# Performance work log

Measured on AMD Instinct MI355X. Metric: run time of the kernel, lower is better.

The kernel has to match this reference:

```python
import jax, jax.numpy as jnp
import numpy as np

L = 2          # conv layers
N = 50000      # nodes
E = 800000     # edges (before self loops)
F_IN = 256     # raw node features
C = 32         # embed features (out_channels per head)
H = 4          # heads
HC = H * C
ED = 1         # edge feature dim
EPS = 1e-5
NEG_SLOPE = 0.2


def _xavier(k, shape):
    fan_in, fan_out = shape[-2], shape[-1]
    lim = float(np.sqrt(6.0 / (fan_in + fan_out)))
    return jax.random.uniform(k, shape, jnp.float32, -lim, lim)


def setup_inputs() -> dict:
    key = jax.random.key(0)
    ks = jax.random.split(key, 12)
    x = jax.random.normal(ks[0], (N, F_IN), jnp.float32)
    src = jax.random.randint(ks[1], (E,), 0, N, dtype=jnp.int32)
    off = jax.random.randint(ks[2], (E,), 1, N, dtype=jnp.int32)
    dst = (src + off) % N  # guarantees no pre-existing self loops (PyG removes then re-adds them)
    edge_index = jnp.stack([src, dst])
    edge_attr = jax.random.normal(ks[3], (E, ED), jnp.float32)
    return {
        "x": x,
        "edge_index": edge_index,
        "edge_attr": edge_attr,
        "W_emb": _xavier(ks[4], (F_IN, C)),
        "b_emb": jnp.zeros((C,), jnp.float32),
        "ln0_w": jnp.ones((C,), jnp.float32),
        "ln0_b": jnp.zeros((C,), jnp.float32),
        "Wl": _xavier(ks[5], (L, C, HC)),
        "bl": jnp.zeros((L, HC), jnp.float32),
        "Wr": _xavier(ks[6], (L, C, HC)),
        "br": jnp.zeros((L, HC), jnp.float32),
        "We": _xavier(ks[7], (L, ED, HC)),
        "att": jax.random.normal(ks[8], (L, H, C), jnp.float32) * 0.1,
        "gat_b": jnp.zeros((L, HC), jnp.float32),
        "ln1_w": jnp.ones((L, HC), jnp.float32),
        "ln1_b": jnp.zeros((L, HC), jnp.float32),
        "lin_w": _xavier(ks[9], (L, HC, C)),
        "lin_b": jnp.zeros((L, C), jnp.float32),
        "ln2_w": jnp.ones((L, C), jnp.float32),
        "ln2_b": jnp.zeros((L, C), jnp.float32),
    }


def _node_ln(x, w, b):
    # torch.nn.LayerNorm over last dim
    mu = jnp.mean(x, axis=-1, keepdims=True)
    xc = x - mu
    var = jnp.mean(xc * xc, axis=-1, keepdims=True)
    return xc / jnp.sqrt(var + EPS) * w + b


def _graph_ln(x, w, b):
    # torch_geometric.nn.norm.LayerNorm, mode='graph': normalize over ALL nodes+features
    mu = jnp.mean(x)
    xc = x - mu
    var = jnp.mean(xc * xc)
    return xc / jnp.sqrt(var + EPS) * w + b


def _gatv2_layer(h, src, dst, ea, Wl, bl, Wr, br, We, att, gat_b):
    n = h.shape[0]
    xl = (h @ Wl + bl).reshape(n, H, C)   # lin_l(x) -> source transform
    xr = (h @ Wr + br).reshape(n, H, C)   # lin_r(x) -> target transform
    e = (ea @ We).reshape(-1, H, C)       # lin_edge(edge_attr), no bias
    z = jax.nn.leaky_relu(xl[src] + xr[dst] + e, NEG_SLOPE)   # [Etot,H,C]
    logits = jnp.einsum("ehc,hc->eh", z, att)                  # [Etot,H]
    # segment softmax over destination nodes (every node has a self loop)
    m = jax.ops.segment_max(logits, dst, num_segments=n)
    ex = jnp.exp(logits - m[dst])
    s = jax.ops.segment_sum(ex, dst, num_segments=n)
    alpha = ex / s[dst]                                        # [Etot,H]
    msg = alpha[..., None] * xl[src]                           # [Etot,H,C]
    out = jax.ops.segment_sum(msg, dst, num_segments=n)        # [N,H,C]
    return out.reshape(n, HC) + gat_b


def reference(x, edge_index, edge_attr, W_emb, b_emb, ln0_w, ln0_b, Wl, bl, Wr, br,
              We, att, gat_b, ln1_w, ln1_b, lin_w, lin_b, ln2_w, ln2_b):
    n = x.shape[0]
    loop = jnp.arange(n, dtype=edge_index.dtype)
    src = jnp.concatenate([edge_index[0], loop])
    dst = jnp.concatenate([edge_index[1], loop])
    ea = jnp.concatenate([edge_attr, jnp.zeros((n, edge_attr.shape[1]), edge_attr.dtype)])  # fill_value=0.0

    # node_embed: Dropout(eval=identity) -> Linear -> LayerNorm -> ReLU
    h = jax.nn.relu(_node_ln(x @ W_emb + b_emb, ln0_w, ln0_b))
    hs = [h]
    for i in range(L):
        g = _gatv2_layer(h, src, dst, ea, Wl[i], bl[i], Wr[i], br[i], We[i], att[i], gat_b[i])
        g = jax.nn.relu(_graph_ln(g, ln1_w[i], ln1_b[i]))     # PyG graph-mode LayerNorm + ReLU
        g = g @ lin_w[i] + lin_b[i]                            # heads>1 projection back to C
        h = jax.nn.relu(_node_ln(g, ln2_w[i], ln2_b[i]))
        hs.append(h)
    # JumpingKnowledge mode='max': elementwise max over layer outputs
    return jnp.max(jnp.stack(hs, axis=0), axis=0)
```

## Files before the change

### kernel.cpp

```cpp
#include <hip/hip_runtime.h>
#include <hip/hip_fp16.h>

constexpr int kNodes = 50000;
constexpr int kNE    = 800000;
constexpr int kFin   = 256;
constexpr int kC     = 32;
constexpr int kH     = 4;
constexpr int kHC    = 128;
constexpr int kTN    = 16;
constexpr int kEmbedBlocks = kNodes / kTN;
constexpr int kTransBlocks = (kNodes + 31) / 32;
constexpr int kHistGS = 256;
constexpr int kReoGS  = 256;
constexpr int kDegBlocks = (kNodes + 255) / 256;
constexpr float kEps   = 1e-5f;
constexpr float kSlope = 0.2f;
constexpr float kL2E   = 1.44269504f;
constexpr float kShift2 = 8.0f * 1.44269504f;

typedef _Float16 f16;
typedef _Float16 f16x2 __attribute__((ext_vector_type(2)));
typedef _Float16 f16x4 __attribute__((ext_vector_type(4)));
struct alignas(16) h8 { f16x2 v[4]; };

__device__ __forceinline__ float fdot2_(f16x2 a, f16x2 b, float c) {
#if __has_builtin(__builtin_amdgcn_fdot2)
    return __builtin_amdgcn_fdot2(a, b, c, false);
#else
    return fmaf((float)a.x, (float)b.x, fmaf((float)a.y, (float)b.y, c));
#endif
}

template<int CTRL>
__device__ __forceinline__ float dpp_add(float v) {
    int x = __builtin_amdgcn_update_dpp(0, __float_as_int(v), CTRL, 0xF, 0xF, true);
    return v + __int_as_float(x);
}
__device__ __forceinline__ float red8(float p) {
    p = dpp_add<0xB1>(p);
    p = dpp_add<0x4E>(p);
    p = dpp_add<0x141>(p);
    return p;
}

__global__ void __launch_bounds__(256) k_prep(
    unsigned* __restrict__ deg, const float* __restrict__ W, f16* __restrict__ Wh,
    const float* __restrict__ linw, f16* __restrict__ lwh, float* __restrict__ stats) {
    int t = threadIdx.x;
    if (blockIdx.x == 0 && t < 4) stats[t] = 0.f;
    if (blockIdx.x < kDegBlocks) {
        int i = blockIdx.x * 256 + t;
        if (i < kNodes) deg[i] = 0u;
        return;
    }
    int bi = blockIdx.x - kDegBlocks;
    if (bi < 32) {
        int i = bi * 256 + t;
        int k = i >> 5, c = i & 31;
        Wh[((k >> 3) * kC + c) * 8 + (k & 7)] = (f16)W[i];
        return;
    }
    bi -= 32;
    int i = bi * 256 + t;
    int l = i >> 12, il = i & 4095;
    int k = il >> 5, c = il & 31;
    lwh[l * 4096 + ((k >> 3) * kC + c) * 8 + (k & 7)] = (f16)linw[i];
}

__global__ void __launch_bounds__(256) k_embed_hist(
    const float* __restrict__ x, const f16* __restrict__ Wh, const float* __restrict__ b,
    const float* __restrict__ lnw, const float* __restrict__ lnb,
    float* __restrict__ h, float* __restrict__ jk,
    const int* __restrict__ dst, int* __restrict__ deg, unsigned short* __restrict__ rank) {
    __shared__ f16 sxh[kTN * kFin];
    __shared__ f16 sWh[kFin / 8 * kC * 8];
    int t = threadIdx.x;
    if (blockIdx.x < kHistGS) {
        const int stride = kHistGS * 256;
        int e = blockIdx.x * 256 + t;
        for (; e + 3 * stride < kNE; e += 4 * stride) {
            int d0 = dst[e], d1 = dst[e + stride], d2 = dst[e + 2 * stride], d3 = dst[e + 3 * stride];
            int r0 = atomicAdd(&deg[d0], 1);
            int r1 = atomicAdd(&deg[d1], 1);
            int r2 = atomicAdd(&deg[d2], 1);
            int r3 = atomicAdd(&deg[d3], 1);
            rank[e] = (unsigned short)r0;
            rank[e + stride] = (unsigned short)r1;
            rank[e + 2 * stride] = (unsigned short)r2;
            rank[e + 3 * stride] = (unsigned short)r3;
        }
        for (; e < kNE; e += stride) {
            int d = dst[e];
            rank[e] = (unsigned short)atomicAdd(&deg[d], 1);
        }
        return;
    }
    int n0 = (blockIdx.x - kHistGS) * kTN;
    {
        const h8* Wg = (const h8*)Wh;
        h8* sW8 = (h8*)sWh;
        for (int i = t; i < kFin * kC / 8; i += 256) sW8[i] = Wg[i];
    }
    const float4* xg4 = (const float4*)(x + (long)n0 * kFin);
    f16x4* sx4 = (f16x4*)sxh;
    for (int i = t; i < kTN * kFin / 4; i += 256) {
        float4 v = xg4[i];
        f16x4 hv; hv.x = (f16)v.x; hv.y = (f16)v.y; hv.z = (f16)v.z; hv.w = (f16)v.w;
        sx4[i] = hv;
    }
    __syncthreads();
    int c = t & 31, n2 = t >> 5;
    const h8* xa = (const h8*)(sxh + n2 * kFin);
    const h8* xb = (const h8*)(sxh + (n2 + 8) * kFin);
    const h8* wr = (const h8*)sWh;
    float a0 = 0.f, a0b = 0.f, a1 = 0.f, a1b = 0.f;
    #pragma unroll 8
    for (int i8 = 0; i8 < kFin / 8; ++i8) {
        h8 xv0 = xa[i8];
        h8 xv1 = xb[i8];
        h8 wv  = wr[i8 * kC + c];
        a0  = fdot2_(xv0.v[0], wv.v[0], a0);
        a0b = fdot2_(xv0.v[1], wv.v[1], a0b);
        a0  = fdot2_(xv0.v[2], wv.v[2], a0);
        a0b = fdot2_(xv0.v[3], wv.v[3], a0b);
        a1  = fdot2_(xv1.v[0], wv.v[0], a1);
        a1b = fdot2_(xv1.v[1], wv.v[1], a1b);
        a1  = fdot2_(xv1.v[2], wv.v[2], a1);
        a1b = fdot2_(xv1.v[3], wv.v[3], a1b);
    }
    float acc0 = a0 + a0b, acc1 = a1 + a1b;
    float bc = b[c], lw = lnw[c], lb = lnb[c];
    {
        float y = acc0 + bc;
        float m = y;
        #pragma unroll
        for (int o = 1; o < 32; o <<= 1) m += __shfl_xor(m, o);
        m *= (1.f / kC);
        float xc = y - m, v = xc * xc;
        #pragma unroll
        for (int o = 1; o < 32; o <<= 1) v += __shfl_xor(v, o);
        v *= (1.f / kC);
        float out = fmaxf(xc * rsqrtf(v + kEps) * lw + lb, 0.f);
        int node = n0 + n2;
        h[node * kC + c] = out;
        jk[node * kC + c] = out;
    }
    {
        float y = acc1 + bc;
        float m = y;
        #pragma unroll
        for (int o = 1; o < 32; o <<= 1) m += __shfl_xor(m, o);
        m *= (1.f / kC);
        float xc = y - m, v = xc * xc;
        #pragma unroll
        for (int o = 1; o < 32; o <<= 1) v += __shfl_xor(v, o);
        v *= (1.f / kC);
        float out = fmaxf(xc * rsqrtf(v + kEps) * lw + lb, 0.f);
        int node = n0 + n2 + 8;
        h[node * kC + c] = out;
        jk[node * kC + c] = out;
    }
}

__device__ __forceinline__ void trans_body(
    int bid, float* s_h, const float* __restrict__ h,
    const float* __restrict__ Wl, const float* __restrict__ bl,
    const float* __restrict__ Wr, const float* __restrict__ br,
    __half* __restrict__ xl, float* __restrict__ xr) {
    int t = threadIdx.x;
    int j = t & 127, hf = t >> 7;
    float wl[kC], wr[kC];
    #pragma unroll
    for (int k = 0; k < kC; ++k) { wl[k] = Wl[k * kHC + j]; wr[k] = Wr[k * kHC + j]; }
    float blj = bl[j], brj = br[j];
    int n0 = bid * 32;
    int nn = min(32, kNodes - n0);
    for (int i = t; i < nn * kC; i += 256) s_h[i] = h[n0 * kC + i];
    __syncthreads();
    int nend = min(nn, hf * 16 + 16);
    for (int n = hf * 16; n < nend; ++n) {
        const float4* h4 = (const float4*)(s_h + n * kC);
        float al = blj, ar = brj;
        #pragma unroll
        for (int kq = 0; kq < 8; ++kq) {
            float4 hv = h4[kq];
            al += hv.x * wl[kq*4] + hv.y * wl[kq*4+1] + hv.z * wl[kq*4+2] + hv.w * wl[kq*4+3];
            ar += hv.x * wr[kq*4] + hv.y * wr[kq*4+1] + hv.z * wr[kq*4+2] + hv.w * wr[kq*4+3];
        }
        long g = (long)(n0 + n) * kHC + j;
        xl[g] = __float2half(al);
        xr[g] = ar;
    }
}

__global__ void __launch_bounds__(256) k_trans_reorder(
    const float* __restrict__ h,
    const float* __restrict__ Wl, const float* __restrict__ bl,
    const float* __restrict__ Wr, const float* __restrict__ br,
    __half* __restrict__ xl, float* __restrict__ xr,
    const int* __restrict__ src, const int* __restrict__ dst, const float* __restrict__ ea,
    const int* __restrict__ rowptr, const unsigned short* __restrict__ rank,
    int2* __restrict__ epack) {
    __shared__ float s_h[32 * kC];
    if (blockIdx.x < kReoGS) {
        const int stride = kReoGS * 256;
        int e = blockIdx.x * 256 + threadIdx.x;
        for (; e + 3 * stride < kNE; e += 4 * stride) {
            int e1 = e + stride, e2 = e + 2 * stride, e3 = e + 3 * stride;
            int d0 = dst[e], d1 = dst[e1], d2 = dst[e2], d3 = dst[e3];
            int r0 = rank[e], r1 = rank[e1], r2 = rank[e2], r3 = rank[e3];
            int p0 = rowptr[d0] + r0, p1 = rowptr[d1] + r1;
            int p2 = rowptr[d2] + r2, p3 = rowptr[d3] + r3;
            epack[p0] = make_int2(src[e],  __float_as_int(ea[e]));
            epack[p1] = make_int2(src[e1], __float_as_int(ea[e1]));
            epack[p2] = make_int2(src[e2], __float_as_int(ea[e2]));
            epack[p3] = make_int2(src[e3], __float_as_int(ea[e3]));
        }
        for (; e < kNE; e += stride) {
            int d = dst[e];
            int pos = rowptr[d] + (int)rank[e];
            epack[pos] = make_int2(src[e], __float_as_int(ea[e]));
        }
        return;
    }
    trans_body(blockIdx.x - kReoGS, s_h, h, Wl, bl, Wr, br, xl, xr);
}

__global__ void __launch_bounds__(256) k_scan1(const int* __restrict__ deg,
                                               int* __restrict__ excl, int* __restrict__ bsum) {
    __shared__ int s[256];
    int t = threadIdx.x;
    int i = blockIdx.x * 256 + t;
    int v = (i < kNodes) ? deg[i] : 0;
    s[t] = v;
    __syncthreads();
    for (int o = 1; o < 256; o <<= 1) {
        int tv = (t >= o) ? s[t - o] : 0;
        __syncthreads();
        s[t] += tv;
        __syncthreads();
    }
    if (i < kNodes) excl[i] = s[t] - v;
    if (t == 255) bsum[blockIdx.x] = s[255];
}

__global__ void __launch_bounds__(256) k_scan2(int* __restrict__ bsum, int nb) {
    __shared__ int s[256];
    int t = threadIdx.x;
    int v = (t < nb) ? bsum[t] : 0;
    s[t] = v;
    __syncthreads();
    for (int o = 1; o < 256; o <<= 1) {
        int tv = (t >= o) ? s[t - o] : 0;
        __syncthreads();
        s[t] += tv;
        __syncthreads();
    }
    if (t < nb) bsum[t] = s[t];
}

__global__ void __launch_bounds__(256) k_scan3(int* __restrict__ excl, const int* __restrict__ bsum) {
    int i = blockIdx.x * 256 + threadIdx.x;
    if (i >= kNodes) return;
    if (blockIdx.x > 0) excl[i] += bsum[blockIdx.x - 1];
}

struct h4 { __half2 a, b; };
template<int U>
__device__ __forceinline__ void gat_batch(
    const int2* __restrict__ epack, int base2, bool slot0, int f,
    const h4* __restrict__ xl4, float4 Wev, float4 xrv, float4 av,
    float& l, float& o0, float& o1, float& o2, float& o3) {
    int2 pa[U], pb[U];
    #pragma unroll
    for (int u = 0; u < U; ++u) {
        pa[u] = epack[base2 + 2 * u];
        pb[u] = epack[base2 + 2 * u + 1];
    }
    h4 xv[U]; float eav[U];
    #pragma unroll
    for (int u = 0; u < U; ++u) {
        int srow = slot0 ? pa[u].x : pb[u].x;
        xv[u] = xl4[(long)srow * 32 + f];
        eav[u] = __int_as_float(slot0 ? pa[u].y : pb[u].y);
    }
    #pragma unroll
    for (int u = 0; u < U; ++u) {
        float2 x01 = __half22float2(xv[u].a), x23 = __half22float2(xv[u].b);
        float a0 = fmaf(eav[u], Wev.x, xrv.x) + x01.x;
        float a1 = fmaf(eav[u], Wev.y, xrv.y) + x01.y;
        float a2 = fmaf(eav[u], Wev.z, xrv.z) + x23.x;
        float a3 = fmaf(eav[u], Wev.w, xrv.w) + x23.y;
        a0 = fmaxf(a0, kSlope * a0); a1 = fmaxf(a1, kSlope * a1);
        a2 = fmaxf(a2, kSlope * a2); a3 = fmaxf(a3, kSlope * a3);
        float pp = red8(a0 * av.x + a1 * av.y + a2 * av.z + a3 * av.w);
        float eu = __builtin_amdgcn_exp2f(pp - kShift2);
        l += eu;
        o0 = fmaf(eu, x01.x, o0); o1 = fmaf(eu, x01.y, o1);
        o2 = fmaf(eu, x23.x, o2); o3 = fmaf(eu, x23.y, o3);
    }
}

__global__ void __launch_bounds__(256) k_edge(
    const int* __restrict__ rowptr, const int* __restrict__ deg,
    const int2* __restrict__ epack,
    const __half* __restrict__ xl, float* __restrict__ xrg,
    const float* __restrict__ We, const float* __restrict__ att,
    const float* __restrict__ gat_b, float* __restrict__ ps, float* __restrict__ pq) {
    int t = threadIdx.x & 63;
    int w = __builtin_amdgcn_readfirstlane(threadIdx.x >> 6);
    int d = blockIdx.x * 4 + w;
    int f = t & 31;
    bool slot0 = (t < 32);
    float em0 = slot0 ? 1.f : 0.f;

    const h4* xl4 = (const h4*)xl;
    long rowq = (long)d * 32;

    float4 xrv = ((const float4*)xrg)[rowq + f];
    float4 Wev = ((const float4*)We)[f];
    float4 av  = ((const float4*)att)[f];
    av.x *= kL2E; av.y *= kL2E; av.z *= kL2E; av.w *= kL2E;
    float4 gb  = ((const float4*)gat_b)[f];

    h4 xs = xl4[rowq + f];
    float2 xs01 = __half22float2(xs.a), xs23 = __half22float2(xs.b);

    float z0 = xs01.x + xrv.x, z1 = xs01.y + xrv.y;
    float z2 = xs23.x + xrv.z, z3 = xs23.y + xrv.w;
    z0 = fmaxf(z0, kSlope * z0); z1 = fmaxf(z1, kSlope * z1);
    z2 = fmaxf(z2, kSlope * z2); z3 = fmaxf(z3, kSlope * z3);
    float p = red8(z0 * av.x + z1 * av.y + z2 * av.z + z3 * av.w);
    float ee = __builtin_amdgcn_exp2f(p - kShift2) * em0;
    float l = ee;
    float o0 = ee * xs01.x, o1 = ee * xs01.y, o2 = ee * xs23.x, o3 = ee * xs23.y;

    int base = rowptr[d], cnt = deg[d];
    int npair = cnt >> 1;
    int e = 0;
    for (; e + 8 <= npair; e += 8)
        gat_batch<8>(epack, base + 2 * e, slot0, f, xl4, Wev, xrv, av, l, o0, o1, o2, o3);
    if (e + 4 <= npair) {
        gat_batch<4>(epack, base + 2 * e, slot0, f, xl4, Wev, xrv, av, l, o0, o1, o2, o3);
        e += 4;
    }
    for (; e < npair; ++e)
        gat_batch<1>(epack, base + 2 * e, slot0, f, xl4, Wev, xrv, av, l, o0, o1, o2, o3);
    if (cnt & 1) {
        int2 ep = epack[base + cnt - 1];
        int srow = ep.x;
        float eav = __int_as_float(ep.y);
        h4 xv = xl4[(long)srow * 32 + f];
        float2 x01 = __half22float2(xv.a), x23 = __half22float2(xv.b);
        float a0 = fmaf(eav, Wev.x, xrv.x) + x01.x;
        float a1 = fmaf(eav, Wev.y, xrv.y) + x01.y;
        float a2 = fmaf(eav, Wev.z, xrv.z) + x23.x;
        float a3 = fmaf(eav, Wev.w, xrv.w) + x23.y;
        a0 = fmaxf(a0, kSlope * a0); a1 = fmaxf(a1, kSlope * a1);
        a2 = fmaxf(a2, kSlope * a2); a3 = fmaxf(a3, kSlope * a3);
        float pp = red8(a0 * av.x + a1 * av.y + a2 * av.z + a3 * av.w);
        float eu = __builtin_amdgcn_exp2f(pp - kShift2) * em0;
        l += eu;
        o0 = fmaf(eu, x01.x, o0); o1 = fmaf(eu, x01.y, o1);
        o2 = fmaf(eu, x23.x, o2); o3 = fmaf(eu, x23.y, o3);
    }
    l  += __shfl_xor(l, 32);
    o0 += __shfl_xor(o0, 32); o1 += __shfl_xor(o1, 32);
    o2 += __shfl_xor(o2, 32); o3 += __shfl_xor(o3, 32);
    float rl = __builtin_amdgcn_rcpf(l);
    float v0 = o0 * rl, v1 = o1 * rl, v2 = o2 * rl, v3 = o3 * rl;
    if (slot0)
        ((float4*)xrg)[rowq + f] = make_float4(v0, v1, v2, v3);
    float vb0 = v0 + gb.x, vb1 = v1 + gb.y, vb2 = v2 + gb.z, vb3 = v3 + gb.w;
    float s = vb0 + vb1 + vb2 + vb3;
    float q = vb0 * vb0 + vb1 * vb1 + vb2 * vb2 + vb3 * vb3;
    #pragma unroll
    for (int mm = 1; mm < 32; mm <<= 1) { s += __shfl_xor(s, mm); q += __shfl_xor(q, mm); }
    if (t == 0) { ps[d] = s; pq[d] = q; }
}

__global__ void __launch_bounds__(1024) k_statsr(
    const float* __restrict__ ps, const float* __restrict__ pq, float* __restrict__ stats) {
    __shared__ float rs[1024], rq[1024];
    int t = threadIdx.x;
    float s = 0.f, q = 0.f;
    for (int i = blockIdx.x * 1024 + t; i < kNodes; i += 8 * 1024) { s += ps[i]; q += pq[i]; }
    rs[t] = s; rq[t] = q;
    __syncthreads();
    for (int o = 512; o > 0; o >>= 1) {
        if (t < o) { rs[t] += rs[t + o]; rq[t] += rq[t + o]; }
        __syncthreads();
    }
    if (t == 0) { atomicAdd(&stats[0], rs[0]); atomicAdd(&stats[1], rq[0]); }
}

__global__ void __launch_bounds__(256) k_post(
    const float* __restrict__ g, const float* __restrict__ gat_b,
    const float* __restrict__ ln1w, const float* __restrict__ ln1b,
    const f16* __restrict__ lwh, const float* __restrict__ linb,
    const float* __restrict__ ln2w, const float* __restrict__ ln2b,
    const float* __restrict__ stats, const float* __restrict__ jk_in,
    float* __restrict__ jk_out, int do_trans,
    const float* __restrict__ Wl, const float* __restrict__ bl,
    const float* __restrict__ Wr, const float* __restrict__ br,
    __half* __restrict__ xl, float* __restrict__ xr) {
    __shared__ __align__(16) char smem[17408];
    float* s_hh  = (float*)smem;
    f16*   s_lwh = (f16*)(smem + 1024);
    f16*   s_vbh = (f16*)(smem + 9216);
    int t = threadIdx.x;
    int n0 = blockIdx.x * 8;
    int j = t & 127;
    const float inv = 1.f / ((float)kNodes * kHC);
    float mean = stats[0] * inv;
    float var  = stats[1] * inv - mean * mean;
    float rstd = rsqrtf(var + kEps);
    {
        const h8* Wg = (const h8*)lwh;
        h8* sW8 = (h8*)s_lwh;
        for (int i = t; i < kHC * kC / 8; i += 256) sW8[i] = Wg[i];
    }
    for (int i = t; i < 8 * kHC; i += 256) {
        int node = n0 + (i >> 7), f = i & 127;
        float a = (g[(long)node * kHC + f] + gat_b[f] - mean) * rstd * ln1w[f] + ln1b[f];
        s_vbh[i] = (f16)fmaxf(a, 0.f);
    }
    __syncthreads();
    int n = t >> 5, c = t & 31;
    int node = n0 + n;
    const h8* vb8 = (const h8*)(s_vbh + n * kHC);
    const h8* w8  = (const h8*)s_lwh;
    float a0 = 0.f, a0b = 0.f;
    #pragma unroll
    for (int k8 = 0; k8 < kHC / 8; ++k8) {
        h8 vv = vb8[k8];
        h8 wv = w8[k8 * kC + c];
        a0  = fdot2_(vv.v[0], wv.v[0], a0);
        a0b = fdot2_(vv.v[1], wv.v[1], a0b);
        a0  = fdot2_(vv.v[2], wv.v[2], a0);
        a0b = fdot2_(vv.v[3], wv.v[3], a0b);
    }
    float acc = linb[c] + a0 + a0b;
    float m = acc;
    #pragma unroll
    for (int mm = 1; mm < 32; mm <<= 1) m += __shfl_xor(m, mm);
    m *= (1.f / kC);
    float dd = acc - m;
    float q = dd * dd;
    #pragma unroll
    for (int mm = 1; mm < 32; mm <<= 1) q += __shfl_xor(q, mm);
    q *= (1.f / kC);
    float out = dd * rsqrtf(q + kEps) * ln2w[c] + ln2b[c];
    out = fmaxf(out, 0.f);
    jk_out[node * kC + c] = fmaxf(jk_in[node * kC + c], out);
    if (!do_trans) return;
    s_hh[n * kC + c] = out;
    __syncthreads();
    f16x2* w2 = (f16x2*)(smem + 1024);
    for (int i = t; i < kC * kHC; i += 256) {
        f16x2 pw; pw.x = (f16)Wl[i]; pw.y = (f16)Wr[i];
        w2[i] = pw;
    }
    __syncthreads();
    float wl[kC], wr[kC];
    #pragma unroll
    for (int k = 0; k < kC; ++k) {
        f16x2 pw = w2[k * kHC + j];
        wl[k] = (float)pw.x; wr[k] = (float)pw.y;
    }
    int hf = t >> 7;
    float blj = bl[j], brj = br[j];
    #pragma unroll
    for (int nn2 = 0; nn2 < 4; ++nn2) {
        int nn = hf * 4 + nn2;
        const float4* h4p = (const float4*)(s_hh + nn * kC);
        float al = blj, ar = brj;
        #pragma unroll
        for (int kq = 0; kq < 8; ++kq) {
            float4 hv = h4p[kq];
            al += hv.x * wl[kq*4] + hv.y * wl[kq*4+1] + hv.z * wl[kq*4+2] + hv.w * wl[kq*4+3];
            ar += hv.x * wr[kq*4] + hv.y * wr[kq*4+1] + hv.z * wr[kq*4+2] + hv.w * wr[kq*4+3];
        }
        long gg = (long)(n0 + nn) * kHC + j;
        xl[gg] = __float2half(al);
        xr[gg] = ar;
    }
}

extern "C" void kernel_launch(void* const* d_in, const int* in_sizes, int n_in,
                              void* d_out, int out_size, void* d_ws, size_t ws_size,
                              hipStream_t stream) {
    (void)in_sizes; (void)n_in; (void)out_size; (void)ws_size;
    const float* x     = (const float*)d_in[0];
    const int*   ei    = (const int*)d_in[1];
    const int*   src   = ei;
    const int*   dst   = ei + kNE;
    const float* ea    = (const float*)d_in[2];
    const float* W_emb = (const float*)d_in[3];
    const float* b_emb = (const float*)d_in[4];
    const float* ln0w  = (const float*)d_in[5];
    const float* ln0b  = (const float*)d_in[6];
    const float* Wl    = (const float*)d_in[7];
    const float* bl    = (const float*)d_in[8];
    const float* Wr    = (const float*)d_in[9];
    const float* br    = (const float*)d_in[10];
    const float* We    = (const float*)d_in[11];
    const float* att   = (const float*)d_in[12];
    const float* gat_b = (const float*)d_in[13];
    const float* ln1w  = (const float*)d_in[14];
    const float* ln1b  = (const float*)d_in[15];
    const float* linw  = (const float*)d_in[16];
    const float* linb  = (const float*)d_in[17];
    const float* ln2w  = (const float*)d_in[18];
    const float* ln2b  = (const float*)d_in[19];

    char* wsb = (char*)d_ws;
    float*  h      = (float*)(wsb);
    float*  jk     = (float*)(wsb +  6400000);
    float*  xrg    = (float*)(wsb + 12800000);
    __half* xl     = (__half*)(wsb + 38400000);
    int2*   epack  = (int2*)(wsb + 51200000);
    int*    deg    = (int*)(wsb + 57600000);
    int*    rowptr = (int*)(wsb + 58000000);
    int*    bsum   = (int*)(wsb + 58200000);
    float*  stats  = (float*)(wsb + 58201024);
    float*  ps     = (float*)(wsb + 58300000);
    float*  pq     = (float*)(wsb + 58500000);
    unsigned short* rank = (unsigned short*)(wsb + 58700000);
    f16*    Wh     = (f16*)(wsb + 60400000);
    f16*    lwh    = (f16*)(wsb + 60420000);

    const int scanBlocks = (kNodes + 255) / 256;
    const int edgeBlocks = kNodes / 4;
    const int postBlocks = kNodes / 8;

    hipLaunchKernelGGL(k_prep, dim3(kDegBlocks + 64), dim3(256), 0, stream,
                       (unsigned*)deg, W_emb, Wh, linw, lwh, stats);
    hipLaunchKernelGGL(k_embed_hist, dim3(kHistGS + kEmbedBlocks), dim3(256), 0, stream,
                       x, Wh, b_emb, ln0w, ln0b, h, jk, dst, deg, rank);
    hipLaunchKernelGGL(k_scan1, dim3(scanBlocks), dim3(256), 0, stream, deg, rowptr, bsum);
    hipLaunchKernelGGL(k_scan2, dim3(1), dim3(256), 0, stream, bsum, scanBlocks);
    hipLaunchKernelGGL(k_scan3, dim3(scanBlocks), dim3(256), 0, stream, rowptr, bsum);
    hipLaunchKernelGGL(k_trans_reorder, dim3(kReoGS + kTransBlocks), dim3(256), 0, stream,
                       h, Wl, bl, Wr, br, xl, xrg,
                       src, dst, ea, rowptr, rank, epack);
    for (int l = 0; l < 2; ++l) {
        hipLaunchKernelGGL(k_edge, dim3(edgeBlocks), dim3(256), 0, stream,
                           rowptr, deg, epack, xl, xrg,
                           We + l * kHC, att + l * kH * kC, gat_b + l * kHC, ps, pq);
        hipLaunchKernelGGL(k_statsr, dim3(8), dim3(1024), 0, stream, ps, pq, stats + 2 * l);
        hipLaunchKernelGGL(k_post, dim3(postBlocks), dim3(256), 0, stream,
                           xrg, gat_b + l * kHC, ln1w + l * kHC, ln1b + l * kHC,
                           lwh + l * kHC * kC, linb + l * kC,
                           ln2w + l * kC, ln2b + l * kC, stats + 2 * l, jk,
                           (l == 1) ? (float*)d_out : jk,
                           (l == 0) ? 1 : 0,
                           Wl + kC * kHC, bl + kHC, Wr + kC * kHC, br + kHC,
                           xl, xrg);
    }
}
```

Measured before the change: 389.4 us.

## Store xr and GAT output in fp16 and fold stats reduction into edge kernel

```diff
diff --git a/kernel.cpp b/kernel.cpp
--- a/kernel.cpp
+++ b/kernel.cpp
@@ -166,7 +166,7 @@
     int bid, float* s_h, const float* __restrict__ h,
     const float* __restrict__ Wl, const float* __restrict__ bl,
     const float* __restrict__ Wr, const float* __restrict__ br,
-    __half* __restrict__ xl, float* __restrict__ xr) {
+    __half* __restrict__ xl, __half* __restrict__ xrh) {
     int t = threadIdx.x;
     int j = t & 127, hf = t >> 7;
     float wl[kC], wr[kC];
@@ -189,7 +189,7 @@
         }
         long g = (long)(n0 + n) * kHC + j;
         xl[g] = __float2half(al);
-        xr[g] = ar;
+        xrh[g] = __float2half(ar);
     }
 }
 
@@ -197,7 +197,7 @@
     const float* __restrict__ h,
     const float* __restrict__ Wl, const float* __restrict__ bl,
     const float* __restrict__ Wr, const float* __restrict__ br,
-    __half* __restrict__ xl, float* __restrict__ xr,
+    __half* __restrict__ xl, __half* __restrict__ xrh,
     const int* __restrict__ src, const int* __restrict__ dst, const float* __restrict__ ea,
     const int* __restrict__ rowptr, const unsigned short* __restrict__ rank,
     int2* __restrict__ epack) {
@@ -223,7 +223,7 @@
         }
         return;
     }
-    trans_body(blockIdx.x - kReoGS, s_h, h, Wl, bl, Wr, br, xl, xr);
+    trans_body(blockIdx.x - kReoGS, s_h, h, Wl, bl, Wr, br, xl, xrh);
 }
 
 __global__ void __launch_bounds__(256) k_scan1(const int* __restrict__ deg,
@@ -304,9 +304,11 @@
 __global__ void __launch_bounds__(256) k_edge(
     const int* __restrict__ rowptr, const int* __restrict__ deg,
     const int2* __restrict__ epack,
-    const __half* __restrict__ xl, float* __restrict__ xrg,
+    const __half* __restrict__ xl, const __half* __restrict__ xrh,
+    __half* __restrict__ gh,
     const float* __restrict__ We, const float* __restrict__ att,
-    const float* __restrict__ gat_b, float* __restrict__ ps, float* __restrict__ pq) {
+    const float* __restrict__ gat_b, float* __restrict__ stats) {
+    __shared__ float s_sq[8];
     int t = threadIdx.x & 63;
     int w = __builtin_amdgcn_readfirstlane(threadIdx.x >> 6);
     int d = blockIdx.x * 4 + w;
@@ -317,7 +319,9 @@
     const h4* xl4 = (const h4*)xl;
     long rowq = (long)d * 32;
 
-    float4 xrv = ((const float4*)xrg)[rowq + f];
+    h4 xr4 = ((const h4*)xrh)[rowq + f];
+    float2 xr01 = __half22float2(xr4.a), xr23 = __half22float2(xr4.b);
+    float4 xrv = make_float4(xr01.x, xr01.y, xr23.x, xr23.y);
     float4 Wev = ((const float4*)We)[f];
     float4 av  = ((const float4*)att)[f];
     av.x *= kL2E; av.y *= kL2E; av.z *= kL2E; av.w *= kL2E;
@@ -369,33 +373,29 @@
     o2 += __shfl_xor(o2, 32); o3 += __shfl_xor(o3, 32);
     float rl = __builtin_amdgcn_rcpf(l);
     float v0 = o0 * rl, v1 = o1 * rl, v2 = o2 * rl, v3 = o3 * rl;
-    if (slot0)
-        ((float4*)xrg)[rowq + f] = make_float4(v0, v1, v2, v3);
+    if (slot0) {
+        h4 gv;
+        gv.a = __float22half2_rn(make_float2(v0, v1));
+        gv.b = __float22half2_rn(make_float2(v2, v3));
+        ((h4*)gh)[rowq + f] = gv;
+    }
     float vb0 = v0 + gb.x, vb1 = v1 + gb.y, vb2 = v2 + gb.z, vb3 = v3 + gb.w;
     float s = vb0 + vb1 + vb2 + vb3;
     float q = vb0 * vb0 + vb1 * vb1 + vb2 * vb2 + vb3 * vb3;
     #pragma unroll
     for (int mm = 1; mm < 32; mm <<= 1) { s += __shfl_xor(s, mm); q += __shfl_xor(q, mm); }
-    if (t == 0) { ps[d] = s; pq[d] = q; }
-}
-
-__global__ void __launch_bounds__(1024) k_statsr(
-    const float* __restrict__ ps, const float* __restrict__ pq, float* __restrict__ stats) {
-    __shared__ float rs[1024], rq[1024];
-    int t = threadIdx.x;
-    float s = 0.f, q = 0.f;
-    for (int i = blockIdx.x * 1024 + t; i < kNodes; i += 8 * 1024) { s += ps[i]; q += pq[i]; }
-    rs[t] = s; rq[t] = q;
-    __syncthreads();
-    for (int o = 512; o > 0; o >>= 1) {
-        if (t < o) { rs[t] += rs[t + o]; rq[t] += rq[t + o]; }
-        __syncthreads();
-    }
-    if (t == 0) { atomicAdd(&stats[0], rs[0]); atomicAdd(&stats[1], rq[0]); }
+    if (t == 0) { s_sq[w * 2] = s; s_sq[w * 2 + 1] = q; }
+    __syncthreads();
+    if (threadIdx.x == 0) {
+        float ss = s_sq[0] + s_sq[2] + s_sq[4] + s_sq[6];
+        float qq = s_sq[1] + s_sq[3] + s_sq[5] + s_sq[7];
+        atomicAdd(&stats[0], ss);
+        atomicAdd(&stats[1], qq);
+    }
 }
 
 __global__ void __launch_bounds__(256) k_post(
-    const float* __restrict__ g, const float* __restrict__ gat_b,
+    const __half* __restrict__ gh, const float* __restrict__ gat_b,
     const float* __restrict__ ln1w, const float* __restrict__ ln1b,
     const f16* __restrict__ lwh, const float* __restrict__ linb,
     const float* __restrict__ ln2w, const float* __restrict__ ln2b,
@@ -403,7 +403,7 @@
     float* __restrict__ jk_out, int do_trans,
     const float* __restrict__ Wl, const float* __restrict__ bl,
     const float* __restrict__ Wr, const float* __restrict__ br,
-    __half* __restrict__ xl, float* __restrict__ xr) {
+    __half* __restrict__ xl, __half* __restrict__ xrh) {
     __shared__ __align__(16) char smem[17408];
     float* s_hh  = (float*)smem;
     f16*   s_lwh = (f16*)(smem + 1024);
@@ -422,7 +422,8 @@
     }
     for (int i = t; i < 8 * kHC; i += 256) {
         int node = n0 + (i >> 7), f = i & 127;
-        float a = (g[(long)node * kHC + f] + gat_b[f] - mean) * rstd * ln1w[f] + ln1b[f];
+        float gv = __half2float(gh[(long)node * kHC + f]);
+        float a = (gv + gat_b[f] - mean) * rstd * ln1w[f] + ln1b[f];
         s_vbh[i] = (f16)fmaxf(a, 0.f);
     }
     __syncthreads();
@@ -483,7 +484,7 @@
         }
         long gg = (long)(n0 + nn) * kHC + j;
         xl[gg] = __float2half(al);
-        xr[gg] = ar;
+        xrh[gg] = __float2half(ar);
     }
 }
 
@@ -517,15 +518,14 @@
     char* wsb = (char*)d_ws;
     float*  h      = (float*)(wsb);
     float*  jk     = (float*)(wsb +  6400000);
-    float*  xrg    = (float*)(wsb + 12800000);
+    __half* xrh    = (__half*)(wsb + 12800000);
+    __half* gh     = (__half*)(wsb + 25600000);
     __half* xl     = (__half*)(wsb + 38400000);
     int2*   epack  = (int2*)(wsb + 51200000);
     int*    deg    = (int*)(wsb + 57600000);
     int*    rowptr = (int*)(wsb + 58000000);
     int*    bsum   = (int*)(wsb + 58200000);
     float*  stats  = (float*)(wsb + 58201024);
-    float*  ps     = (float*)(wsb + 58300000);
-    float*  pq     = (float*)(wsb + 58500000);
     unsigned short* rank = (unsigned short*)(wsb + 58700000);
     f16*    Wh     = (f16*)(wsb + 60400000);
     f16*    lwh    = (f16*)(wsb + 60420000);
@@ -542,20 +542,20 @@
     hipLaunchKernelGGL(k_scan2, dim3(1), dim3(256), 0, stream, bsum, scanBlocks);
     hipLaunchKernelGGL(k_scan3, dim3(scanBlocks), dim3(256), 0, stream, rowptr, bsum);
     hipLaunchKernelGGL(k_trans_reorder, dim3(kReoGS + kTransBlocks), dim3(256), 0, stream,
-                       h, Wl, bl, Wr, br, xl, xrg,
+                       h, Wl, bl, Wr, br, xl, xrh,
                        src, dst, ea, rowptr, rank, epack);
     for (int l = 0; l < 2; ++l) {
         hipLaunchKernelGGL(k_edge, dim3(edgeBlocks), dim3(256), 0, stream,
-                           rowptr, deg, epack, xl, xrg,
-                           We + l * kHC, att + l * kH * kC, gat_b + l * kHC, ps, pq);
-        hipLaunchKernelGGL(k_statsr, dim3(8), dim3(1024), 0, stream, ps, pq, stats + 2 * l);
+                           rowptr, deg, epack, xl, xrh, gh,
+                           We + l * kHC, att + l * kH * kC, gat_b + l * kHC,
+                           stats + 2 * l);
         hipLaunchKernelGGL(k_post, dim3(postBlocks), dim3(256), 0, stream,
-                           xrg, gat_b + l * kHC, ln1w + l * kHC, ln1b + l * kHC,
+                           gh, gat_b + l * kHC, ln1w + l * kHC, ln1b + l * kHC,
                            lwh + l * kHC * kC, linb + l * kC,
                            ln2w + l * kC, ln2b + l * kC, stats + 2 * l, jk,
                            (l == 1) ? (float*)d_out : jk,
                            (l == 0) ? 1 : 0,
                            Wl + kC * kHC, bl + kHC, Wr + kC * kHC, br + kHC,
-                           xl, xrg);
-    }
-}
+                           xl, xrh);
+    }
+}
```

New measurement: 921.5 us. +136.6%, slower.
